# Performance work log

Hardware: AMD Instinct MI355X
Metric: run time of the kernel (lower is better)

## Reference

```python
import jax, jax.numpy as jnp
import numpy as np

WS = (2, 7, 7)   # window size (d, h, w)
SS = (1, 3, 3)   # shift size
EPS = 1e-5


def _rel_pos_index(ws):
    d, h, w = np.arange(ws[0]), np.arange(ws[1]), np.arange(ws[2])
    coords = np.stack(np.meshgrid(d, h, w, indexing='ij'))        # (3, wd, wh, ww)
    flat = coords.reshape(3, -1)                                   # (3, N)
    rel = flat[:, :, None] - flat[:, None, :]                      # (3, N, N)
    rel = rel.transpose(1, 2, 0).astype(np.int64)                  # (N, N, 3)
    rel[:, :, 0] += ws[0] - 1
    rel[:, :, 1] += ws[1] - 1
    rel[:, :, 2] += ws[2] - 1
    rel[:, :, 0] *= (2 * ws[1] - 1) * (2 * ws[2] - 1)
    rel[:, :, 1] *= 2 * ws[2] - 1
    return rel.sum(-1)                                             # (N, N)


def _window_partition(x, ws):
    B, D, H, W, C = x.shape
    x = x.reshape(B, D // ws[0], ws[0], H // ws[1], ws[1], W // ws[2], ws[2], C)
    return x.transpose(0, 1, 3, 5, 2, 4, 6, 7).reshape(-1, ws[0] * ws[1] * ws[2], C)


def _window_reverse(win, ws, B, D, H, W):
    x = win.reshape(B, D // ws[0], H // ws[1], W // ws[2], ws[0], ws[1], ws[2], -1)
    return x.transpose(0, 1, 4, 2, 5, 3, 6, 7).reshape(B, D, H, W, -1)


def _attn_mask(D, H, W, ws, ss):
    img = np.zeros((1, D, H, W, 1), np.float32)
    cnt = 0
    for dsl in (slice(None, -ws[0]), slice(-ws[0], -ss[0]), slice(-ss[0], None)):
        for hsl in (slice(None, -ws[1]), slice(-ws[1], -ss[1]), slice(-ss[1], None)):
            for wsl in (slice(None, -ws[2]), slice(-ws[2], -ss[2]), slice(-ss[2], None)):
                img[:, dsl, hsl, wsl, :] = cnt
                cnt += 1
    mw = _window_partition(img, ws)[..., 0]                        # (nW, N)
    am = mw[:, None, :] - mw[:, :, None]                           # (nW, N, N)
    return np.where(am != 0, np.float32(-100.0), np.float32(0.0))


def _ln(x, g, b):
    m = x.mean(-1, keepdims=True)
    v = ((x - m) ** 2).mean(-1, keepdims=True)
    return (x - m) / jnp.sqrt(v + EPS) * g + b


def setup_inputs():
    key = jax.random.key(0)
    B, D, H, W, C = 2, 8, 56, 56, 256
    nH, hidden = 8, 1024
    ks = jax.random.split(key, 8)
    s = 0.02
    inp = {
        'x': jax.random.normal(ks[0], (B, D, H, W, C), jnp.float32),
        'qkv_w': jax.random.normal(ks[1], (3 * C, C), jnp.float32) * s,
        'qkv_b': jnp.zeros((3 * C,), jnp.float32),
        'proj_w': jax.random.normal(ks[2], (C, C), jnp.float32) * s,
        'proj_b': jnp.zeros((C,), jnp.float32),
        'rpb_table': jax.random.normal(ks[3], (3 * 13 * 13, nH), jnp.float32) * s,
        'ln1_g': jnp.ones((C,), jnp.float32),
        'ln1_b': jnp.zeros((C,), jnp.float32),
        'ln2_g': jnp.ones((C,), jnp.float32),
        'ln2_b': jnp.zeros((C,), jnp.float32),
        'fc1_w': jax.random.normal(ks[4], (hidden, C), jnp.float32) * s,
        'fc1_b': jnp.zeros((hidden,), jnp.float32),
        'fc2_w': jax.random.normal(ks[5], (C, hidden), jnp.float32) * s,
        'fc2_b': jnp.zeros((C,), jnp.float32),
        'rel_idx': jnp.asarray(_rel_pos_index(WS), jnp.int32),
        'attn_mask': jnp.asarray(_attn_mask(D, H, W, WS, SS)),
        'num_heads': nH,
    }
    return inp


def reference(x, qkv_w, qkv_b, proj_w, proj_b, rpb_table, ln1_g, ln1_b, ln2_g,
              ln2_b, fc1_w, fc1_b, fc2_w, fc2_b, rel_idx, attn_mask, num_heads):
    B, D, H, W, C = x.shape
    N = WS[0] * WS[1] * WS[2]
    hd = C // num_heads
    scale = hd ** (-0.5)

    shortcut = x
    h = _ln(x, ln1_g, ln1_b)
    # cyclic shift
    h = jnp.roll(h, shift=(-SS[0], -SS[1], -SS[2]), axis=(1, 2, 3))
    win = _window_partition(h, WS)                                 # (B_, N, C)

    qkv = win @ qkv_w.T + qkv_b                                    # (B_, N, 3C)
    qkv = qkv.reshape(-1, N, 3, num_heads, hd).transpose(2, 0, 3, 1, 4)
    q, k, v = qkv[0] * scale, qkv[1], qkv[2]                       # (B_, nH, N, hd)

    attn = jnp.einsum('bhid,bhjd->bhij', q, k)                     # (B_, nH, N, N)
    bias = rpb_table[rel_idx.reshape(-1)].reshape(N, N, num_heads).transpose(2, 0, 1)
    attn = attn + bias[None]
    nW = attn_mask.shape[0]
    attn = attn.reshape(B, nW, num_heads, N, N) + attn_mask[None, :, None]
    attn = jax.nn.softmax(attn.reshape(-1, num_heads, N, N), axis=-1)

    out = jnp.einsum('bhij,bhjd->bhid', attn, v)                   # (B_, nH, N, hd)
    out = out.transpose(0, 2, 1, 3).reshape(-1, N, C)
    out = out @ proj_w.T + proj_b

    xr = _window_reverse(out, WS, B, D, H, W)
    xr = jnp.roll(xr, shift=SS, axis=(1, 2, 3))                    # reverse shift
    x = shortcut + xr

    h2 = _ln(x, ln2_g, ln2_b)
    m = jax.nn.gelu(h2 @ fc1_w.T + fc1_b, approximate=False)
    m = m @ fc2_w.T + fc2_b
    return x + m
```

## Files before the change

kernel.cpp:

```cpp
#include <hip/hip_runtime.h>
#include <hip/hip_bf16.h>
#include <math.h>

#define B_  2
#define D_  8
#define H_  56
#define W_  56
#define C_  256
#define NH_ 8
#define HD_ 32
#define N_  98
#define NWIN_TOT 512
#define TOK (B_*D_*H_*W_)
#define HID 1024

typedef short bf16x8 __attribute__((ext_vector_type(8)));
typedef float f32x4  __attribute__((ext_vector_type(4)));

__device__ __forceinline__ ushort f2b(float f) {
    union { float f; unsigned u; } v; v.f = f;
    unsigned r = v.u + 0x7fff + ((v.u >> 16) & 1);
    return (ushort)(r >> 16);
}
__device__ __forceinline__ float b2f(ushort h) {
    union { unsigned u; float f; } v; v.u = ((unsigned)h) << 16;
    return v.f;
}

__device__ __forceinline__ void glds16(const void* gsrc, void* lds_dst) {
    __builtin_amdgcn_global_load_lds(
        (const __attribute__((address_space(1))) unsigned int*)gsrc,
        (__attribute__((address_space(3))) unsigned int*)lds_dst,
        16, 0, 0);
}

__device__ __forceinline__ int tok_of_winrow(int r) {
    int wid  = r / N_;
    int n    = r - wid * N_;
    int b    = wid >> 8;
    int rem  = wid & 255;
    int di   = rem >> 6;
    int hi   = (rem >> 3) & 7;
    int wi   = rem & 7;
    int wd   = n / 49;
    int rem2 = n - wd * 49;
    int wh   = rem2 / 7;
    int ww   = rem2 - wh * 7;
    int d = di * 2 + wd + 1; if (d >= D_) d -= D_;
    int h = hi * 7 + wh + 3; if (h >= H_) h -= H_;
    int w = wi * 7 + ww + 3; if (w >= W_) w -= W_;
    return ((b * D_ + d) * H_ + h) * W_ + w;
}

__device__ __forceinline__ float gelu_exact(float x) {
    return 0.5f * x * (1.0f + erff(x * 0.70710678118654752f));
}

template<bool GATHER>
__global__ __launch_bounds__(256)
void ln_kernel(const float* __restrict__ x, const float* __restrict__ g,
               const float* __restrict__ bta, ushort* __restrict__ out, int nrows) {
    int wave = blockIdx.x * 4 + (threadIdx.x >> 6);
    int lane = threadIdx.x & 63;
    if (wave >= nrows) return;
    int srow = GATHER ? tok_of_winrow(wave) : wave;
    float4 v = ((const float4*)(x + (size_t)srow * C_))[lane];
    float s  = v.x + v.y + v.z + v.w;
    float ss = v.x*v.x + v.y*v.y + v.z*v.z + v.w*v.w;
    #pragma unroll
    for (int o = 32; o; o >>= 1) { s += __shfl_xor(s, o); ss += __shfl_xor(ss, o); }
    float mean = s * (1.0f / C_);
    float var  = ss * (1.0f / C_) - mean * mean;
    float rstd = rsqrtf(var + 1e-5f);
    float4 gg = ((const float4*)g)[lane];
    float4 bb = ((const float4*)bta)[lane];
    ushort4 o4;
    o4.x = f2b((v.x - mean) * rstd * gg.x + bb.x);
    o4.y = f2b((v.y - mean) * rstd * gg.y + bb.y);
    o4.z = f2b((v.z - mean) * rstd * gg.z + bb.z);
    o4.w = f2b((v.w - mean) * rstd * gg.w + bb.w);
    ((ushort4*)(out + (size_t)wave * C_))[lane] = o4;
}

#define TB2_WORDS (8 * 8 * 7 * 14 * 64)
__global__ void tbl_kernel(const int* __restrict__ rel_idx,
                           const float* __restrict__ rpb,
                           const float* __restrict__ mask,
                           uint* __restrict__ Tb2) {
    int idx = blockIdx.x * blockDim.x + threadIdx.x;
    if (idx >= TB2_WORDS) return;
    int lane = idx & 63;
    int t    = idx >> 6;
    int nq   = t % 14;  int t2 = t / 14;
    int mi   = t2 % 7;  int ph = t2 / 7;
    int pat  = ph >> 3, hh = ph & 7;
    int nj   = nq >> 1, q = nq & 1;
    int lrow = lane & 15, lgrp = lane >> 4;
    int j  = nj * 16 + lrow;
    int i0 = mi * 16 + lgrp * 4 + q * 2;
    int di = (pat & 1) ? 3 : 0, hi = (pat & 2) ? 7 : 0, wi = (pat & 4) ? 7 : 0;
    int rep = di * 64 + hi * 8 + wi;
    float lo = -1e30f, hv = -1e30f;
    if (j < N_) {
        if (i0 < N_)
            lo = rpb[rel_idx[i0 * N_ + j] * NH_ + hh] + mask[(size_t)rep * (N_*N_) + i0 * N_ + j];
        if (i0 + 1 < N_)
            hv = rpb[rel_idx[(i0+1) * N_ + j] * NH_ + hh] + mask[(size_t)rep * (N_*N_) + (i0+1) * N_ + j];
    }
    Tb2[idx] = (uint)f2b(lo) | ((uint)f2b(hv) << 16);
}

__global__ void f2b4_kernel(const float* __restrict__ s0, ushort* __restrict__ d0, int n0,
                            const float* __restrict__ s1, ushort* __restrict__ d1, int n1,
                            const float* __restrict__ s2, ushort* __restrict__ d2, int n2,
                            const float* __restrict__ s3, ushort* __restrict__ d3, int n3) {
    const float* s; ushort* d; int n;
    switch (blockIdx.y) {
        case 0: s = s0; d = d0; n = n0; break;
        case 1: s = s1; d = d1; n = n1; break;
        case 2: s = s2; d = d2; n = n2; break;
        default: s = s3; d = d3; n = n3; break;
    }
    int i = (blockIdx.x * blockDim.x + threadIdx.x) * 4;
    if (i >= n) return;
    float4 v = *(const float4*)(s + i);
    ushort4 o; o.x = f2b(v.x); o.y = f2b(v.y); o.z = f2b(v.z); o.w = f2b(v.w);
    *(ushort4*)(d + i) = o;
}

template<int MODE>
__global__ __launch_bounds__(256)
void gemm_bf16(const ushort* __restrict__ A, const ushort* __restrict__ Wm,
               const float* __restrict__ bias, void* __restrict__ Cout,
               const void* __restrict__ resid, int M, int K, int Nout) {
    __shared__ __align__(16) char lds[32768];
    char* ldsA = lds;
    char* ldsB = lds + 16384;
    const int tid  = threadIdx.x;
    const int wv   = tid >> 6, lane = tid & 63;
    const int m0   = blockIdx.x * 128, n0 = blockIdx.y * 128;
    const int wrow = (wv >> 1) * 64, wcol = (wv & 1) * 64;
    const int lr8  = lane >> 3, lc = lane & 7;

    f32x4 acc[4][4] = {};

    const ushort* Ag[4]; const ushort* Bg[4];
    #pragma unroll
    for (int i = 0; i < 4; ++i) {
        int row = (wv * 4 + i) * 8 + lr8;
        int gc  = lc ^ (row & 7);
        Ag[i] = A  + (size_t)(m0 + row) * K + gc * 8;
        Bg[i] = Wm + (size_t)(n0 + row) * K + gc * 8;
    }

    for (int k0 = 0; k0 < K; k0 += 64) {
        #pragma unroll
        for (int i = 0; i < 4; ++i) {
            glds16(Ag[i] + k0, ldsA + (wv * 4 + i) * 1024);
            glds16(Bg[i] + k0, ldsB + (wv * 4 + i) * 1024);
        }
        __syncthreads();
        #pragma unroll
        for (int kk = 0; kk < 2; ++kk) {
            bf16x8 af[4], bfr[4];
            #pragma unroll
            for (int i = 0; i < 4; ++i) {
                int r = wrow + i * 16 + (lane & 15);
                int c = (lane >> 4) + kk * 4;
                af[i]  = *(const bf16x8*)(ldsA + r * 128 + ((c ^ (r & 7)) * 16));
                int r2 = wcol + i * 16 + (lane & 15);
                bfr[i] = *(const bf16x8*)(ldsB + r2 * 128 + ((c ^ (r2 & 7)) * 16));
            }
            #pragma unroll
            for (int i = 0; i < 4; ++i)
                #pragma unroll
                for (int j = 0; j < 4; ++j)
                    acc[i][j] = __builtin_amdgcn_mfma_f32_16x16x32_bf16(af[i], bfr[j], acc[i][j], 0, 0, 0);
        }
        __syncthreads();
    }

    int colg[4]; float bv[4];
    #pragma unroll
    for (int j = 0; j < 4; ++j) {
        colg[j] = n0 + wcol + j * 16 + (lane & 15);
        bv[j]   = bias[colg[j]];
    }
    #pragma unroll
    for (int i = 0; i < 4; ++i) {
        #pragma unroll
        for (int r = 0; r < 4; ++r) {
            int rowg = m0 + wrow + i * 16 + ((lane >> 4) << 2) + r;
            int tok = (MODE == 1) ? tok_of_winrow(rowg) : rowg;
            #pragma unroll
            for (int j = 0; j < 4; ++j) {
                float v = acc[i][j][r] + bv[j];
                if (MODE == 0) {
                    ((ushort*)Cout)[(size_t)rowg * Nout + colg[j]] = f2b(v);
                } else if (MODE == 1) {
                    v += ((const float*)resid)[(size_t)tok * C_ + colg[j]];
                    ((float*)Cout)[(size_t)tok * C_ + colg[j]] = v;
                } else if (MODE == 2) {
                    ((ushort*)Cout)[(size_t)rowg * Nout + colg[j]] = f2b(gelu_exact(v));
                } else {
                    v += ((const float*)resid)[(size_t)rowg * Nout + colg[j]];
                    ((float*)Cout)[(size_t)rowg * Nout + colg[j]] = v;
                }
            }
        }
    }
}

#define KOFF 0
#define VOFF 7168
#define POFF 15360
#define SMEM_BYTES 32768
__global__ __launch_bounds__(256)
void attn_mfma(const ushort* __restrict__ qkv, const uint* __restrict__ Tb2,
               ushort* __restrict__ attn_out) {
    __shared__ __align__(16) char smem[SMEM_BYTES];
    ushort (*Pl)[16][136] = (ushort (*)[16][136])(smem + POFF);
    const int b    = blockIdx.x;
    const int wid  = (b & 7) + ((b >> 6) << 3);
    const int hh   = (b >> 3) & 7;
    const int tid  = threadIdx.x;
    const int wv   = tid >> 6, lane = tid & 63;
    const int lrow = lane & 15, lgrp = lane >> 4;
    const float scale = 0.17677669529663687f;

    const ushort* base = qkv + (size_t)wid * N_ * 768 + hh * 32;
    const int rem = wid & 255;
    const int pat = (((rem >> 6) == 3) ? 1 : 0) | ((((rem >> 3) & 7) == 7) ? 2 : 0)
                  | (((rem & 7) == 7) ? 4 : 0);
    const uint* tb2 = Tb2 + (size_t)((pat * 8 + hh) * 7) * 14 * 64 + lane;

    {
        uint4 z = {0, 0, 0, 0};
        uint4* l4 = (uint4*)(smem + 14336);
        for (int i = tid; i < (SMEM_BYTES - 14336) / 16; i += 256) l4[i] = z;
    }
    __syncthreads();

    #pragma unroll
    for (int sect = 0; sect < 2; ++sect) {
        char* dstbase = smem + sect * 7168;
        const ushort* src = base + 256 + sect * 256;
        for (int c = tid; c < 448; c += 256) {
            int r = c >> 2; if (r > 97) r = 97;
            int cc = c & 3;
            glds16(src + (size_t)r * 768 + ((cc ^ (r & 3)) * 8), dstbase + c * 16);
        }
    }
    __syncthreads();

    const int swz = (lgrp ^ (lrow & 3)) << 4;

    bf16x8 kf[7];
    #pragma unroll
    for (int nj = 0; nj < 7; ++nj)
        kf[nj] = *(const bf16x8*)(smem + KOFF + (nj * 16 + lrow) * 64 + swz);

    bf16x8 vf[2][4];
    #pragma unroll
    for (int dt = 0; dt < 2; ++dt)
        #pragma unroll
        for (int kt = 0; kt < 4; ++kt) {
            bf16x8 tmp;
            #pragma unroll
            for (int t = 0; t < 8; ++t) {
                int R = kt * 32 + lgrp * 8 + t;
                int q = dt * 2 + (lrow >> 3);
                tmp[t] = *(const short*)(smem + VOFF + R * 64 +
                                         ((q ^ (t & 3)) << 4) + ((lrow & 7) << 1));
            }
            vf[dt][kt] = tmp;
        }

    for (int mi = wv; mi < 7; mi += 4) {
        const int ibase = mi * 16;

        uint tw[14];
        const uint* tbm = tb2 + mi * 14 * 64;
        #pragma unroll
        for (int u = 0; u < 14; ++u) tw[u] = tbm[u * 64];

        bf16x8 qf = *(const bf16x8*)(base + (size_t)(ibase + lrow) * 768 + lgrp * 8);

        f32x4 s[7];
        #pragma unroll
        for (int nj = 0; nj < 7; ++nj) {
            f32x4 z = {0.f, 0.f, 0.f, 0.f};
            s[nj] = __builtin_amdgcn_mfma_f32_16x16x32_bf16(qf, kf[nj], z, 0, 0, 0);
        }

        #pragma unroll
        for (int nj = 0; nj < 7; ++nj) {
            #pragma unroll
            for (int r = 0; r < 4; ++r) {
                uint w = tw[nj * 2 + (r >> 1)];
                ushort hb = (r & 1) ? (ushort)(w >> 16) : (ushort)(w & 0xffff);
                s[nj][r] = s[nj][r] * scale + b2f(hb);
            }
        }

        float rinv[4];
        #pragma unroll
        for (int r = 0; r < 4; ++r) {
            float acc = 0.f;
            #pragma unroll
            for (int nj = 0; nj < 7; ++nj) {
                float p = __expf(s[nj][r]);
                s[nj][r] = p;
                acc += p;
            }
            #pragma unroll
            for (int o = 1; o < 16; o <<= 1) acc += __shfl_xor(acc, o);
            rinv[r] = 1.f / acc;
        }

        #pragma unroll
        for (int nj = 0; nj < 7; ++nj)
            #pragma unroll
            for (int r = 0; r < 4; ++r)
                Pl[wv][lgrp * 4 + r][nj * 16 + lrow] = f2b(s[nj][r] * rinv[r]);

        f32x4 o0 = {0.f, 0.f, 0.f, 0.f}, o1 = {0.f, 0.f, 0.f, 0.f};
        #pragma unroll
        for (int kt = 0; kt < 4; ++kt) {
            bf16x8 pf = *(const bf16x8*)(&Pl[wv][lrow][kt * 32 + lgrp * 8]);
            o0 = __builtin_amdgcn_mfma_f32_16x16x32_bf16(pf, vf[0][kt], o0, 0, 0, 0);
            o1 = __builtin_amdgcn_mfma_f32_16x16x32_bf16(pf, vf[1][kt], o1, 0, 0, 0);
        }

        #pragma unroll
        for (int r = 0; r < 4; ++r) {
            int i = ibase + lgrp * 4 + r;
            if (i < N_) {
                size_t rb = ((size_t)(wid * N_ + i)) * C_ + hh * 32;
                attn_out[rb + lrow]      = f2b(o0[r]);
                attn_out[rb + 16 + lrow] = f2b(o1[r]);
            }
        }
    }
}

extern "C" void kernel_launch(void* const* d_in, const int* in_sizes, int n_in,
                              void* d_out, int out_size, void* d_ws, size_t ws_size,
                              hipStream_t stream) {
    const float* x      = (const float*)d_in[0];
    const float* qkv_w  = (const float*)d_in[1];
    const float* qkv_b  = (const float*)d_in[2];
    const float* proj_w = (const float*)d_in[3];
    const float* proj_b = (const float*)d_in[4];
    const float* rpb    = (const float*)d_in[5];
    const float* ln1_g  = (const float*)d_in[6];
    const float* ln1_b  = (const float*)d_in[7];
    const float* ln2_g  = (const float*)d_in[8];
    const float* ln2_b  = (const float*)d_in[9];
    const float* fc1_w  = (const float*)d_in[10];
    const float* fc1_b  = (const float*)d_in[11];
    const float* fc2_w  = (const float*)d_in[12];
    const float* fc2_b  = (const float*)d_in[13];
    const int*   rel_idx= (const int*)d_in[14];
    const float* mask   = (const float*)d_in[15];
    float* out = (float*)d_out;

    char* ws = (char*)d_ws;
    ushort* regionA = (ushort*)ws;
    ushort* regionB = (ushort*)(ws + (size_t)TOK * HID * 2);
    ushort* wq  = (ushort*)(ws + (size_t)TOK * HID * 2 + (size_t)TOK * C_ * 2);
    ushort* wp  = wq + 768 * 256;
    ushort* w1  = wp + 256 * 256;
    ushort* w2  = w1 + HID * 256;
    uint*   Tb2 = (uint*)(w2 + 256 * HID);

    tbl_kernel<<<(TB2_WORDS + 255) / 256, 256, 0, stream>>>(rel_idx, rpb, mask, Tb2);
    {
        dim3 g(256, 4);
        f2b4_kernel<<<g, 256, 0, stream>>>(qkv_w, wq, 768 * 256,
                                           proj_w, wp, 256 * 256,
                                           fc1_w, w1, HID * 256,
                                           fc2_w, w2, 256 * HID);
    }

    ln_kernel<true><<<TOK / 4, 256, 0, stream>>>(x, ln1_g, ln1_b, regionB, TOK);

    {
        dim3 g(TOK / 128, 768 / 128);
        gemm_bf16<0><<<g, 256, 0, stream>>>(regionB, wq, qkv_b, regionA, nullptr, TOK, 256, 768);
    }

    attn_mfma<<<NWIN_TOT * NH_, 256, 0, stream>>>(regionA, Tb2, regionB);

    {
        dim3 g(TOK / 128, 256 / 128);
        gemm_bf16<1><<<g, 256, 0, stream>>>(regionB, wp, proj_b, out, x, TOK, 256, 256);
    }

    ln_kernel<false><<<TOK / 4, 256, 0, stream>>>(out, ln2_g, ln2_b, regionB, TOK);

    {
        dim3 g(TOK / 128, HID / 128);
        gemm_bf16<2><<<g, 256, 0, stream>>>(regionB, w1, fc1_b, regionA, nullptr, TOK, 256, HID);
    }

    {
        dim3 g(TOK / 128, 256 / 128);
        gemm_bf16<3><<<g, 256, 0, stream>>>(regionA, w2, fc2_b, out, out, TOK, HID, 256);
    }
}
```

Before: 258.2 us.

## Replace LDS-staged GEMM with direct-from-global MFMA operand loads

The shared-memory GEMM, with its swizzled LDS tiles and barriers, is replaced by a kernel where each wave loads its MFMA A and B fragments straight from global memory. Each block covers 64 rows by 256 columns, and the four waves share the A rows through cache rather than LDS. This removes LDS traffic and the __syncthreads barriers. In exchange, global and L2 load traffic rises, loads cannot overlap with MFMA through staging, and the per-lane 16-byte loads are strided by row, which may coalesce poorly.

```diff
diff --git a/kernel.cpp b/kernel.cpp
--- a/kernel.cpp
+++ b/kernel.cpp
@@ -130,67 +130,52 @@
 
 template<int MODE>
 __global__ __launch_bounds__(256)
-void gemm_bf16(const ushort* __restrict__ A, const ushort* __restrict__ Wm,
-               const float* __restrict__ bias, void* __restrict__ Cout,
-               const void* __restrict__ resid, int M, int K, int Nout) {
-    __shared__ __align__(16) char lds[32768];
-    char* ldsA = lds;
-    char* ldsB = lds + 16384;
+void gemm_direct(const ushort* __restrict__ A, const ushort* __restrict__ Wm,
+                 const float* __restrict__ bias, void* __restrict__ Cout,
+                 const void* __restrict__ resid, int M, int K, int Nout) {
     const int tid  = threadIdx.x;
     const int wv   = tid >> 6, lane = tid & 63;
-    const int m0   = blockIdx.x * 128, n0 = blockIdx.y * 128;
-    const int wrow = (wv >> 1) * 64, wcol = (wv & 1) * 64;
-    const int lr8  = lane >> 3, lc = lane & 7;
+    const int lrow = lane & 15, lgrp = lane >> 4;
+    const int m0   = blockIdx.y * 64;
+    const int n0   = blockIdx.x * 256 + wv * 64;
 
     f32x4 acc[4][4] = {};
 
-    const ushort* Ag[4]; const ushort* Bg[4];
+    const ushort* Ap[4]; const ushort* Bp[4];
     #pragma unroll
     for (int i = 0; i < 4; ++i) {
-        int row = (wv * 4 + i) * 8 + lr8;
-        int gc  = lc ^ (row & 7);
-        Ag[i] = A  + (size_t)(m0 + row) * K + gc * 8;
-        Bg[i] = Wm + (size_t)(n0 + row) * K + gc * 8;
-    }
-
-    for (int k0 = 0; k0 < K; k0 += 64) {
-        #pragma unroll
-        for (int i = 0; i < 4; ++i) {
-            glds16(Ag[i] + k0, ldsA + (wv * 4 + i) * 1024);
-            glds16(Bg[i] + k0, ldsB + (wv * 4 + i) * 1024);
-        }
-        __syncthreads();
-        #pragma unroll
-        for (int kk = 0; kk < 2; ++kk) {
+        Ap[i] = A  + (size_t)(m0 + i * 16 + lrow) * K + lgrp * 8;
+        Bp[i] = Wm + (size_t)(n0 + i * 16 + lrow) * K + lgrp * 8;
+    }
+
+    for (int k0 = 0; k0 < K; k0 += 256) {
+        #pragma unroll
+        for (int kk = 0; kk < 8; ++kk) {
+            const int ko = k0 + kk * 32;
             bf16x8 af[4], bfr[4];
             #pragma unroll
-            for (int i = 0; i < 4; ++i) {
-                int r = wrow + i * 16 + (lane & 15);
-                int c = (lane >> 4) + kk * 4;
-                af[i]  = *(const bf16x8*)(ldsA + r * 128 + ((c ^ (r & 7)) * 16));
-                int r2 = wcol + i * 16 + (lane & 15);
-                bfr[i] = *(const bf16x8*)(ldsB + r2 * 128 + ((c ^ (r2 & 7)) * 16));
-            }
+            for (int i = 0; i < 4; ++i) af[i]  = *(const bf16x8*)(Ap[i] + ko);
+            #pragma unroll
+            for (int j = 0; j < 4; ++j) bfr[j] = *(const bf16x8*)(Bp[j] + ko);
             #pragma unroll
             for (int i = 0; i < 4; ++i)
                 #pragma unroll
                 for (int j = 0; j < 4; ++j)
                     acc[i][j] = __builtin_amdgcn_mfma_f32_16x16x32_bf16(af[i], bfr[j], acc[i][j], 0, 0, 0);
         }
-        __syncthreads();
     }
 
     int colg[4]; float bv[4];
     #pragma unroll
     for (int j = 0; j < 4; ++j) {
-        colg[j] = n0 + wcol + j * 16 + (lane & 15);
+        colg[j] = n0 + j * 16 + lrow;
         bv[j]   = bias[colg[j]];
     }
     #pragma unroll
     for (int i = 0; i < 4; ++i) {
         #pragma unroll
         for (int r = 0; r < 4; ++r) {
-            int rowg = m0 + wrow + i * 16 + ((lane >> 4) << 2) + r;
+            int rowg = m0 + i * 16 + lgrp * 4 + r;
             int tok = (MODE == 1) ? tok_of_winrow(rowg) : rowg;
             #pragma unroll
             for (int j = 0; j < 4; ++j) {
@@ -386,26 +371,26 @@
     ln_kernel<true><<<TOK / 4, 256, 0, stream>>>(x, ln1_g, ln1_b, regionB, TOK);
 
     {
-        dim3 g(TOK / 128, 768 / 128);
-        gemm_bf16<0><<<g, 256, 0, stream>>>(regionB, wq, qkv_b, regionA, nullptr, TOK, 256, 768);
+        dim3 g(768 / 256, TOK / 64);
+        gemm_direct<0><<<g, 256, 0, stream>>>(regionB, wq, qkv_b, regionA, nullptr, TOK, 256, 768);
     }
 
     attn_mfma<<<NWIN_TOT * NH_, 256, 0, stream>>>(regionA, Tb2, regionB);
 
     {
-        dim3 g(TOK / 128, 256 / 128);
-        gemm_bf16<1><<<g, 256, 0, stream>>>(regionB, wp, proj_b, out, x, TOK, 256, 256);
+        dim3 g(1, TOK / 64);
+        gemm_direct<1><<<g, 256, 0, stream>>>(regionB, wp, proj_b, out, x, TOK, 256, 256);
     }
 
     ln_kernel<false><<<TOK / 4, 256, 0, stream>>>(out, ln2_g, ln2_b, regionB, TOK);
 
     {
-        dim3 g(TOK / 128, HID / 128);
-        gemm_bf16<2><<<g, 256, 0, stream>>>(regionB, w1, fc1_b, regionA, nullptr, TOK, 256, HID);
-    }
-
-    {
-        dim3 g(TOK / 128, 256 / 128);
-        gemm_bf16<3><<<g, 256, 0, stream>>>(regionA, w2, fc2_b, out, out, TOK, HID, 256);
-    }
-}
+        dim3 g(HID / 256, TOK / 64);
+        gemm_direct<2><<<g, 256, 0, stream>>>(regionB, w1, fc1_b, regionA, nullptr, TOK, 256, HID);
+    }
+
+    {
+        dim3 g(1, TOK / 64);
+        gemm_direct<3><<<g, 256, 0, stream>>>(regionA, w2, fc2_b, out, out, TOK, HID, 256);
+    }
+}
```

Result: slower. 454.1 us (+75.8%).
